# Performance work log

Hardware: AMD Instinct MI355X
Metric: run time of the kernel (lower is better)

## Reference

```python
import jax, jax.numpy as jnp
import numpy as np

FILTER_LEN = 32
SCALE = float(np.sqrt(10 ** (-15 / 10)))  # expected_SI_power_dB = -15


def _fir_valid(x, w):
    """Valid cross-correlation along W axis. x: [B,H,W,1], w: [L] -> [B,H,W-L+1,1].
    Matches Keras Conv2D(kernel_size=(1,L), padding='valid') (cross-correlation)."""
    B, H, W, _ = x.shape
    L = w.shape[0]
    xr = x.reshape(B * H, W, 1)
    k = w.reshape(L, 1, 1)  # (spatial, in, out)
    y = jax.lax.conv_general_dilated(xr, k, window_strides=(1,), padding='VALID',
                                     dimension_numbers=('NWC', 'WIO', 'NWC'))
    return y.reshape(B, H, W - L + 1, 1)


def setup_inputs() -> dict:
    key = jax.random.key(0)
    ks = jax.random.split(key, 10)
    B, H, W = 16, 1, 262144
    f32 = jnp.float32
    return {
        'x_real': jax.random.normal(ks[0], (B, H, W, 1), f32),
        'x_imag': jax.random.normal(ks[1], (B, H, W, 1), f32),
        'w1_pre': jax.random.normal(ks[2], (1, 8), f32) * 0.5,
        'w2_pre': jax.random.normal(ks[3], (8, 1), f32) * 0.5,
        'w_fir_r': jax.random.normal(ks[4], (FILTER_LEN,), f32) * 0.1,
        'w_fir_i': jax.random.normal(ks[5], (FILTER_LEN,), f32) * 0.1,
        'w1_post': jax.random.normal(ks[6], (1, 8), f32) * 0.5,
        'b1_post': jax.random.normal(ks[7], (8,), f32) * 0.1,
        'w2_post': jax.random.normal(ks[8], (8, 1), f32) * 0.5,
        'b2_post': jax.random.normal(ks[9], (1,), f32) * 0.1,
    }


def reference(x_real, x_imag, w1_pre, w2_pre, w_fir_r, w_fir_i,
              w1_post, b1_post, w2_post, b2_post):
    # --- pre nonlinearity on magnitude (1x1 conv MLP: 1 -> 8 tanh -> 1) ---
    x_mag = jnp.sqrt(x_real * x_real + x_imag * x_imag)      # [B,H,W,1]
    x_phase = jnp.arctan2(x_imag, x_real)                    # [B,H,W,1]
    h = jnp.tanh(jnp.einsum('bhwc,cf->bhwf', x_mag, w1_pre))  # [B,H,W,8]
    m = jnp.einsum('bhwf,fc->bhwc', h, w2_pre)               # [B,H,W,1]
    xh_r = m * jnp.cos(x_phase)
    xh_i = m * jnp.sin(x_phase)
    # --- complex FIR (length-32, valid) via 4 real convs ---
    zr = _fir_valid(xh_r, w_fir_r) - _fir_valid(xh_i, w_fir_i)
    zi = _fir_valid(xh_i, w_fir_r) + _fir_valid(xh_r, w_fir_i)
    # --- post nonlinearity on magnitude (1x1 conv MLP: 1 -> 8 relu -> 1) ---
    z_mag = jnp.sqrt(zr * zr + zi * zi)
    z_phase = jnp.arctan2(zi, zr)
    g = jax.nn.relu(jnp.einsum('bhwc,cf->bhwf', z_mag, w1_post) + b1_post)
    zm = jnp.einsum('bhwf,fc->bhwc', g, w2_post) + b2_post
    yr = SCALE * zm * jnp.cos(z_phase)
    yi = SCALE * zm * jnp.sin(z_phase)
    # complex output represented as [real, imag] on last axis: [B,H,W-31,2]
    return jnp.concatenate([yr, yi], axis=-1)
```

## Files before the change

kernel.cpp:

```cpp
#include <hip/hip_runtime.h>

#define WIDTH  262144
#define OUTW   (WIDTH - 31)
#define WTILE  512
#define NSW    560
#define SCALE_V 0.17782794100389229f

#define TBL_N    1024
#define TBL_MAX  10.0f
#define TBL_SCL  (TBL_N / TBL_MAX)

typedef _Float16 half8  __attribute__((ext_vector_type(8)));
typedef _Float16 half4v __attribute__((ext_vector_type(4)));
typedef float    floatx4 __attribute__((ext_vector_type(4)));

__device__ __forceinline__ float wload(const float* __restrict__ w, int t) {
    return (t >= 0 && t < 32) ? w[t] : 0.0f;
}

#define MFMA16(A, B, C) __builtin_amdgcn_mfma_f32_16x16x32_f16((A), (B), (C), 0, 0, 0)

__device__ __forceinline__ float s_of_mag(float mag, const float* w1, const float* w2) {
    if (mag == 0.0f) {
        float s = 0.f;
#pragma unroll
        for (int f = 0; f < 8; ++f) s = fmaf(w2[f], w1[f], s);
        return s;
    }
    float m = 0.f;
#pragma unroll
    for (int f = 0; f < 8; ++f) m = fmaf(w2[f], tanhf(w1[f] * mag), m);
    return m / mag;
}

__global__ void fill_s_table(const float* __restrict__ w1_pre,
                             const float* __restrict__ w2_pre,
                             float2* __restrict__ tbl)
{
    const int i = blockIdx.x * 256 + threadIdx.x;
    if (i >= TBL_N) return;
    float w1[8], w2[8];
#pragma unroll
    for (int f = 0; f < 8; ++f) { w1[f] = w1_pre[f]; w2[f] = w2_pre[f]; }
    const float m0 = (float)i       * (1.0f / TBL_SCL);
    const float m1 = (float)(i + 1) * (1.0f / TBL_SCL);
    const float s0 = s_of_mag(m0, w1, w2);
    const float s1 = s_of_mag(m1, w1, w2);
    tbl[i] = make_float2(s0, s1 - s0);
}

__global__ __launch_bounds__(256, 4) void fused_hammer_mfma(
    const float* __restrict__ xr_g,   const float* __restrict__ xi_g,
    const float* __restrict__ w1_pre, const float* __restrict__ w2_pre,
    const float* __restrict__ wfr,    const float* __restrict__ wfi,
    const float* __restrict__ w1_post,const float* __restrict__ b1_post,
    const float* __restrict__ w2_post,const float* __restrict__ b2_post,
    const float2* __restrict__ tbl_g,
    float* __restrict__ out)
{
    __shared__ __align__(16) _Float16 s_rh[4][NSW];
    __shared__ __align__(16) _Float16 s_rl[4][NSW];
    __shared__ __align__(16) _Float16 s_ih[4][NSW];
    __shared__ __align__(16) _Float16 s_il[4][NSW];
    __shared__ __align__(16) float2   s_tab[TBL_N];

    const int tid    = threadIdx.x;
    const int lane   = tid & 63;
    const int wv     = tid >> 6;
    const int brow   = blockIdx.y;
    const long rowbase = (long)brow * WIDTH;
    const int wbase  = blockIdx.x * 4096 + wv * 1024;

    const int g0 = min(wbase       + 4 * lane, WIDTH - 4);
    const int g1 = min(wbase + 256 + 4 * lane, WIDTH - 4);
    float4 p_r0 = *(const float4*)(xr_g + rowbase + g0);
    float4 p_i0 = *(const float4*)(xi_g + rowbase + g0);
    float4 p_r1 = *(const float4*)(xr_g + rowbase + g1);
    float4 p_i1 = *(const float4*)(xi_g + rowbase + g1);

    {
        const float4* src = (const float4*)tbl_g;
#pragma unroll
        for (int q = 0; q < 2; ++q) {
            const int idx = 2 * tid + q;
            ((float4*)s_tab)[idx] = src[idx];
        }
    }

    float w1p[8], b1p[8], w2p[8];
#pragma unroll
    for (int f = 0; f < 8; ++f) { w1p[f] = w1_post[f]; b1p[f] = b1_post[f]; w2p[f] = w2_post[f]; }
    const float b2p = b2_post[0];

    const int jA = lane & 15;
    const int kg = lane >> 4;
    half8 A1r_h, A1r_l, A1mi_h, A1mi_l, A1i_h, A1i_l, A2r_h, A2r_l, A2i_h, A2i_l;
#pragma unroll
    for (int jj = 0; jj < 8; ++jj) {
        const int k  = 8 * kg + jj;
        const int t1 = k - jA;
        const float wr1 = wload(wfr, t1);
        const float wi1 = wload(wfi, t1);
        const int t2 = (k < 16) ? (k + 32 - jA) : (k + 16 - jA);
        const float wr2 = wload(wfr, t2);
        const float wi2 = wload(wfi, t2);
        const float a2r = (k < 16) ? wr2 : -wi2;
        const float a2i = (k < 16) ? wi2 : wr2;
        _Float16 h;
        h = (_Float16)wr1;   A1r_h[jj]  = h; A1r_l[jj]  = (_Float16)(wr1 - (float)h);
        h = (_Float16)(-wi1);A1mi_h[jj] = h; A1mi_l[jj] = (_Float16)(-wi1 - (float)h);
        h = (_Float16)wi1;   A1i_h[jj]  = h; A1i_l[jj]  = (_Float16)(wi1 - (float)h);
        h = (_Float16)a2r;   A2r_h[jj]  = h; A2r_l[jj]  = (_Float16)(a2r - (float)h);
        h = (_Float16)a2i;   A2i_h[jj]  = h; A2i_l[jj]  = (_Float16)(a2i - (float)h);
    }

    __syncthreads();

    const bool row_aligned = ((brow & 1) == 0);

#define STAGE4(VR, VI, P)                                                     \
    do {                                                                      \
        const float* vrf = &(VR).x;                                           \
        const float* vif = &(VI).x;                                           \
        half4v rh_, rl_, ih_, il_;                                            \
        _Pragma("unroll")                                                     \
        for (int e = 0; e < 4; ++e) {                                         \
            const float r  = vrf[e], im = vif[e];                             \
            const float sq  = fmaf(r, r, im * im);                            \
            const float mag = __builtin_sqrtf(sq);                            \
            const float t   = fminf(mag * TBL_SCL, (float)(TBL_N - 2) + 0.999f); \
            const int   i0  = (int)t;                                         \
            const float frac = t - (float)i0;                                 \
            const float2 en = s_tab[i0];                                      \
            const float s   = fmaf(frac, en.y, en.x);                         \
            const float xhr = s * r;                                          \
            const float xhi = s * im;                                         \
            const _Float16 hr = (_Float16)xhr;                                \
            const _Float16 hi = (_Float16)xhi;                                \
            rh_[e] = hr; rl_[e] = (_Float16)(xhr - (float)hr);                \
            ih_[e] = hi; il_[e] = (_Float16)(xhi - (float)hi);                \
        }                                                                     \
        *(half4v*)&s_rh[wv][4 * (P)] = rh_;                                   \
        *(half4v*)&s_rl[wv][4 * (P)] = rl_;                                   \
        *(half4v*)&s_ih[wv][4 * (P)] = ih_;                                   \
        *(half4v*)&s_il[wv][4 * (P)] = il_;                                   \
    } while (0)

#pragma unroll
    for (int q = 0; q < 2; ++q) {
        const int wstart = wbase + q * WTILE;

        float4 h_r, h_i;
        if (lane < 12) {
            const int g2 = min(wstart + 512 + 4 * lane, WIDTH - 4);
            h_r = *(const float4*)(xr_g + rowbase + g2);
            h_i = *(const float4*)(xi_g + rowbase + g2);
        }

        STAGE4(p_r0, p_i0, lane);
        STAGE4(p_r1, p_i1, 64 + lane);

        if (q == 0) {
            const int n0 = min(wbase + 512       + 4 * lane, WIDTH - 4);
            const int n1 = min(wbase + 512 + 256 + 4 * lane, WIDTH - 4);
            p_r0 = *(const float4*)(xr_g + rowbase + n0);
            p_i0 = *(const float4*)(xi_g + rowbase + n0);
            p_r1 = *(const float4*)(xr_g + rowbase + n1);
            p_i1 = *(const float4*)(xi_g + rowbase + n1);
        }

        if (lane < 12) STAGE4(h_r, h_i, 128 + lane);

        asm volatile("s_waitcnt lgkmcnt(0)" ::: "memory");

#pragma unroll
        for (int tt = 0; tt < 2; ++tt) {
            const int base_o = 256 * tt;
            const int i1 = base_o + 16 * jA + 8 * kg;
            const half8 Bxr_h = *(const half8*)&s_rh[wv][i1];
            const half8 Bxi_h = *(const half8*)&s_ih[wv][i1];
            const half8 Bxr_l = *(const half8*)&s_rl[wv][i1];
            const half8 Bxi_l = *(const half8*)&s_il[wv][i1];
            const int i2 = base_o + 16 * jA + 32 + 8 * (kg & 1);
            const _Float16* srcH = (kg < 2) ? s_rh[wv] : s_ih[wv];
            const _Float16* srcL = (kg < 2) ? s_rl[wv] : s_il[wv];
            const half8 Bmx_h = *(const half8*)&srcH[i2];
            const half8 Bmx_l = *(const half8*)&srcL[i2];

            floatx4 accr = {0.f, 0.f, 0.f, 0.f};
            floatx4 acci = {0.f, 0.f, 0.f, 0.f};
            accr = MFMA16(A1r_h,  Bxr_h, accr);  acci = MFMA16(A1i_h,  Bxr_h, acci);
            accr = MFMA16(A1mi_h, Bxi_h, accr);  acci = MFMA16(A1r_h,  Bxi_h, acci);
            accr = MFMA16(A2r_h,  Bmx_h, accr);  acci = MFMA16(A2i_h,  Bmx_h, acci);
            accr = MFMA16(A1r_h,  Bxr_l, accr);  acci = MFMA16(A1i_h,  Bxr_l, acci);
            accr = MFMA16(A1mi_h, Bxi_l, accr);  acci = MFMA16(A1r_h,  Bxi_l, acci);
            accr = MFMA16(A2r_h,  Bmx_l, accr);  acci = MFMA16(A2i_h,  Bmx_l, acci);
            accr = MFMA16(A1r_l,  Bxr_h, accr);  acci = MFMA16(A1i_l,  Bxr_h, acci);
            accr = MFMA16(A1mi_l, Bxi_h, accr);  acci = MFMA16(A1r_l,  Bxi_h, acci);
            accr = MFMA16(A2r_l,  Bmx_h, accr);  acci = MFMA16(A2i_l,  Bmx_h, acci);

            const int obase = wstart + base_o + 16 * jA + 4 * kg;
            float ox[8];
#pragma unroll
            for (int r = 0; r < 4; ++r) {
                const float zr  = accr[r], zi = acci[r];
                const float zsq = fmaf(zr, zr, zi * zi);
                const float rs  = (zsq > 0.f) ? __builtin_amdgcn_rsqf(zsq) : 0.f;
                const float zmag = zsq * rs;
                float zm = b2p;
#pragma unroll
                for (int f = 0; f < 8; ++f) {
                    const float gfv = fmaf(zmag, w1p[f], b1p[f]);
                    zm = fmaf(fmaxf(gfv, 0.f), w2p[f], zm);
                }
                const float t = SCALE_V * zm * rs;
                ox[2 * r]     = (zsq > 0.f) ? t * zr : SCALE_V * zm;
                ox[2 * r + 1] = t * zi;
            }
            float* po = &out[((long)brow * OUTW + obase) * 2];
            if (obase + 3 < OUTW) {
                if (row_aligned) {
                    *(float4*)(po)     = make_float4(ox[0], ox[1], ox[2], ox[3]);
                    *(float4*)(po + 4) = make_float4(ox[4], ox[5], ox[6], ox[7]);
                } else {
#pragma unroll
                    for (int r = 0; r < 4; ++r)
                        *(float2*)(po + 2 * r) = make_float2(ox[2 * r], ox[2 * r + 1]);
                }
            } else {
#pragma unroll
                for (int r = 0; r < 4; ++r)
                    if (obase + r < OUTW)
                        *(float2*)(po + 2 * r) = make_float2(ox[2 * r], ox[2 * r + 1]);
            }
        }
    }
#undef STAGE4
}

extern "C" void kernel_launch(void* const* d_in, const int* in_sizes, int n_in,
                              void* d_out, int out_size, void* d_ws, size_t ws_size,
                              hipStream_t stream) {
    float2* tbl = (float2*)d_ws;
    fill_s_table<<<dim3((TBL_N + 255) / 256), 256, 0, stream>>>(
        (const float*)d_in[2], (const float*)d_in[3], tbl);

    dim3 grid(64, 16);
    fused_hammer_mfma<<<grid, 256, 0, stream>>>(
        (const float*)d_in[0], (const float*)d_in[1],
        (const float*)d_in[2], (const float*)d_in[3],
        (const float*)d_in[4], (const float*)d_in[5],
        (const float*)d_in[6], (const float*)d_in[7],
        (const float*)d_in[8], (const float*)d_in[9],
        tbl,
        (float*)d_out);
}
```

Measured before the change: 111.2 us.

## Fuse table build into main kernel and halve per-block work

Drops the separate table-fill kernel launch. Each block now builds the magnitude lookup table in shared memory using a fast exp2/rcp tanh, and precomputes fp16 hi/lo FIR weight splits in shared memory. Each wave now handles a single 512-wide tile instead of two, so the grid doubles to 128x16 and the launch-bounds occupancy hint rises to 5. This removes a launch and the global table read, but every block repeats the 1025-entry table computation and the prefetch overlap between tiles is lost.

```diff
diff --git a/kernel.cpp b/kernel.cpp
--- a/kernel.cpp
+++ b/kernel.cpp
@@ -5,6 +5,7 @@
 #define WTILE  512
 #define NSW    560
 #define SCALE_V 0.17782794100389229f
+#define LOG2E_X2 2.8853900817779268f
 
 #define TBL_N    1024
 #define TBL_MAX  10.0f
@@ -14,10 +15,6 @@
 typedef _Float16 half4v __attribute__((ext_vector_type(4)));
 typedef float    floatx4 __attribute__((ext_vector_type(4)));
 
-__device__ __forceinline__ float wload(const float* __restrict__ w, int t) {
-    return (t >= 0 && t < 32) ? w[t] : 0.0f;
-}
-
 #define MFMA16(A, B, C) __builtin_amdgcn_mfma_f32_16x16x32_f16((A), (B), (C), 0, 0, 0)
 
 __device__ __forceinline__ float s_of_mag(float mag, const float* w1, const float* w2) {
@@ -29,68 +26,69 @@
     }
     float m = 0.f;
 #pragma unroll
-    for (int f = 0; f < 8; ++f) m = fmaf(w2[f], tanhf(w1[f] * mag), m);
+    for (int f = 0; f < 8; ++f) {
+        const float e2 = __builtin_amdgcn_exp2f(LOG2E_X2 * w1[f] * mag);
+        const float th = 1.0f - 2.0f * __builtin_amdgcn_rcpf(e2 + 1.0f);
+        m = fmaf(w2[f], th, m);
+    }
     return m / mag;
 }
 
-__global__ void fill_s_table(const float* __restrict__ w1_pre,
-                             const float* __restrict__ w2_pre,
-                             float2* __restrict__ tbl)
-{
-    const int i = blockIdx.x * 256 + threadIdx.x;
-    if (i >= TBL_N) return;
-    float w1[8], w2[8];
-#pragma unroll
-    for (int f = 0; f < 8; ++f) { w1[f] = w1_pre[f]; w2[f] = w2_pre[f]; }
-    const float m0 = (float)i       * (1.0f / TBL_SCL);
-    const float m1 = (float)(i + 1) * (1.0f / TBL_SCL);
-    const float s0 = s_of_mag(m0, w1, w2);
-    const float s1 = s_of_mag(m1, w1, w2);
-    tbl[i] = make_float2(s0, s1 - s0);
-}
-
-__global__ __launch_bounds__(256, 4) void fused_hammer_mfma(
+__global__ __launch_bounds__(256, 5) void fused_hammer_mfma(
     const float* __restrict__ xr_g,   const float* __restrict__ xi_g,
     const float* __restrict__ w1_pre, const float* __restrict__ w2_pre,
     const float* __restrict__ wfr,    const float* __restrict__ wfi,
     const float* __restrict__ w1_post,const float* __restrict__ b1_post,
     const float* __restrict__ w2_post,const float* __restrict__ b2_post,
-    const float2* __restrict__ tbl_g,
     float* __restrict__ out)
 {
     __shared__ __align__(16) _Float16 s_rh[4][NSW];
     __shared__ __align__(16) _Float16 s_rl[4][NSW];
     __shared__ __align__(16) _Float16 s_ih[4][NSW];
     __shared__ __align__(16) _Float16 s_il[4][NSW];
-    __shared__ __align__(16) float2   s_tab[TBL_N];
+    __shared__ __align__(16) float    s_tab[TBL_N + 1];
+    __shared__ __align__(16) _Float16 s_wrh[32], s_wrl[32], s_wih[32], s_wil[32];
 
     const int tid    = threadIdx.x;
     const int lane   = tid & 63;
     const int wv     = tid >> 6;
     const int brow   = blockIdx.y;
     const long rowbase = (long)brow * WIDTH;
-    const int wbase  = blockIdx.x * 4096 + wv * 1024;
-
-    const int g0 = min(wbase       + 4 * lane, WIDTH - 4);
-    const int g1 = min(wbase + 256 + 4 * lane, WIDTH - 4);
-    float4 p_r0 = *(const float4*)(xr_g + rowbase + g0);
-    float4 p_i0 = *(const float4*)(xi_g + rowbase + g0);
-    float4 p_r1 = *(const float4*)(xr_g + rowbase + g1);
-    float4 p_i1 = *(const float4*)(xi_g + rowbase + g1);
+    const int wstart = blockIdx.x * 2048 + wv * WTILE;
+
+    const int g0 = min(wstart       + 4 * lane, WIDTH - 4);
+    const int g1 = min(wstart + 256 + 4 * lane, WIDTH - 4);
+    float4 r0 = *(const float4*)(xr_g + rowbase + g0);
+    float4 i0 = *(const float4*)(xi_g + rowbase + g0);
+    float4 r1 = *(const float4*)(xr_g + rowbase + g1);
+    float4 i1 = *(const float4*)(xi_g + rowbase + g1);
+    float4 r2, i2;
+    if (lane < 12) {
+        const int g2 = min(wstart + 512 + 4 * lane, WIDTH - 4);
+        r2 = *(const float4*)(xr_g + rowbase + g2);
+        i2 = *(const float4*)(xi_g + rowbase + g2);
+    }
 
     {
-        const float4* src = (const float4*)tbl_g;
-#pragma unroll
-        for (int q = 0; q < 2; ++q) {
-            const int idx = 2 * tid + q;
-            ((float4*)s_tab)[idx] = src[idx];
-        }
+        float w1v[8], w2v[8];
+#pragma unroll
+        for (int f = 0; f < 8; ++f) { w1v[f] = w1_pre[f]; w2v[f] = w2_pre[f]; }
+        for (int i = tid; i <= TBL_N; i += 256)
+            s_tab[i] = s_of_mag((float)i * (1.0f / TBL_SCL), w1v, w2v);
+    }
+    if (tid < 32) {
+        const float wr = wfr[tid], wi = wfi[tid];
+        const _Float16 wrh = (_Float16)wr, wih = (_Float16)wi;
+        s_wrh[tid] = wrh; s_wrl[tid] = (_Float16)(wr - (float)wrh);
+        s_wih[tid] = wih; s_wil[tid] = (_Float16)(wi - (float)wih);
     }
 
     float w1p[8], b1p[8], w2p[8];
 #pragma unroll
     for (int f = 0; f < 8; ++f) { w1p[f] = w1_post[f]; b1p[f] = b1_post[f]; w2p[f] = w2_post[f]; }
     const float b2p = b2_post[0];
+
+    __syncthreads();
 
     const int jA = lane & 15;
     const int kg = lane >> 4;
@@ -99,22 +97,24 @@
     for (int jj = 0; jj < 8; ++jj) {
         const int k  = 8 * kg + jj;
         const int t1 = k - jA;
-        const float wr1 = wload(wfr, t1);
-        const float wi1 = wload(wfi, t1);
+        const bool v1 = (t1 >= 0);
+        const int x1 = max(t1, 0);
+        const _Float16 z = (_Float16)0.f;
+        const _Float16 wr1h = v1 ? s_wrh[x1] : z, wr1l = v1 ? s_wrl[x1] : z;
+        const _Float16 wi1h = v1 ? s_wih[x1] : z, wi1l = v1 ? s_wil[x1] : z;
         const int t2 = (k < 16) ? (k + 32 - jA) : (k + 16 - jA);
-        const float wr2 = wload(wfr, t2);
-        const float wi2 = wload(wfi, t2);
-        const float a2r = (k < 16) ? wr2 : -wi2;
-        const float a2i = (k < 16) ? wi2 : wr2;
-        _Float16 h;
-        h = (_Float16)wr1;   A1r_h[jj]  = h; A1r_l[jj]  = (_Float16)(wr1 - (float)h);
-        h = (_Float16)(-wi1);A1mi_h[jj] = h; A1mi_l[jj] = (_Float16)(-wi1 - (float)h);
-        h = (_Float16)wi1;   A1i_h[jj]  = h; A1i_l[jj]  = (_Float16)(wi1 - (float)h);
-        h = (_Float16)a2r;   A2r_h[jj]  = h; A2r_l[jj]  = (_Float16)(a2r - (float)h);
-        h = (_Float16)a2i;   A2i_h[jj]  = h; A2i_l[jj]  = (_Float16)(a2i - (float)h);
-    }
-
-    __syncthreads();
+        const bool v2 = (t2 <= 31);
+        const int x2 = min(t2, 31);
+        const _Float16 wr2h = v2 ? s_wrh[x2] : z, wr2l = v2 ? s_wrl[x2] : z;
+        const _Float16 wi2h = v2 ? s_wih[x2] : z, wi2l = v2 ? s_wil[x2] : z;
+        A1r_h[jj]  = wr1h;  A1r_l[jj]  = wr1l;
+        A1mi_h[jj] = -wi1h; A1mi_l[jj] = -wi1l;
+        A1i_h[jj]  = wi1h;  A1i_l[jj]  = wi1l;
+        A2r_h[jj]  = (k < 16) ? wr2h : -wi2h;
+        A2r_l[jj]  = (k < 16) ? wr2l : -wi2l;
+        A2i_h[jj]  = (k < 16) ? wi2h : wr2h;
+        A2i_l[jj]  = (k < 16) ? wi2l : wr2l;
+    }
 
     const bool row_aligned = ((brow & 1) == 0);
 
@@ -128,11 +128,12 @@
             const float r  = vrf[e], im = vif[e];                             \
             const float sq  = fmaf(r, r, im * im);                            \
             const float mag = __builtin_sqrtf(sq);                            \
-            const float t   = fminf(mag * TBL_SCL, (float)(TBL_N - 2) + 0.999f); \
+            const float t   = fminf(mag * TBL_SCL, (float)TBL_N - 0.001f);    \
             const int   i0  = (int)t;                                         \
             const float frac = t - (float)i0;                                 \
-            const float2 en = s_tab[i0];                                      \
-            const float s   = fmaf(frac, en.y, en.x);                         \
+            const float sa = s_tab[i0];                                       \
+            const float sb = s_tab[i0 + 1];                                   \
+            const float s  = fmaf(frac, sb - sa, sa);                         \
             const float xhr = s * r;                                          \
             const float xhi = s * im;                                         \
             const _Float16 hr = (_Float16)xhr;                                \
@@ -146,93 +147,71 @@
         *(half4v*)&s_il[wv][4 * (P)] = il_;                                   \
     } while (0)
 
-#pragma unroll
-    for (int q = 0; q < 2; ++q) {
-        const int wstart = wbase + q * WTILE;
-
-        float4 h_r, h_i;
-        if (lane < 12) {
-            const int g2 = min(wstart + 512 + 4 * lane, WIDTH - 4);
-            h_r = *(const float4*)(xr_g + rowbase + g2);
-            h_i = *(const float4*)(xi_g + rowbase + g2);
+    STAGE4(r0, i0, lane);
+    STAGE4(r1, i1, 64 + lane);
+    if (lane < 12) STAGE4(r2, i2, 128 + lane);
+
+    asm volatile("s_waitcnt lgkmcnt(0)" ::: "memory");
+
+#pragma unroll
+    for (int tt = 0; tt < 2; ++tt) {
+        const int base_o = 256 * tt;
+        const int i1x = base_o + 16 * jA + 8 * kg;
+        const half8 Bxr_h = *(const half8*)&s_rh[wv][i1x];
+        const half8 Bxi_h = *(const half8*)&s_ih[wv][i1x];
+        const half8 Bxr_l = *(const half8*)&s_rl[wv][i1x];
+        const half8 Bxi_l = *(const half8*)&s_il[wv][i1x];
+        const int i2x = base_o + 16 * jA + 32 + 8 * (kg & 1);
+        const _Float16* srcH = (kg < 2) ? s_rh[wv] : s_ih[wv];
+        const _Float16* srcL = (kg < 2) ? s_rl[wv] : s_il[wv];
+        const half8 Bmx_h = *(const half8*)&srcH[i2x];
+        const half8 Bmx_l = *(const half8*)&srcL[i2x];
+
+        floatx4 accr = {0.f, 0.f, 0.f, 0.f};
+        floatx4 acci = {0.f, 0.f, 0.f, 0.f};
+        accr = MFMA16(A1r_h,  Bxr_h, accr);  acci = MFMA16(A1i_h,  Bxr_h, acci);
+        accr = MFMA16(A1mi_h, Bxi_h, accr);  acci = MFMA16(A1r_h,  Bxi_h, acci);
+        accr = MFMA16(A2r_h,  Bmx_h, accr);  acci = MFMA16(A2i_h,  Bmx_h, acci);
+        accr = MFMA16(A1r_h,  Bxr_l, accr);  acci = MFMA16(A1i_h,  Bxr_l, acci);
+        accr = MFMA16(A1mi_h, Bxi_l, accr);  acci = MFMA16(A1r_h,  Bxi_l, acci);
+        accr = MFMA16(A2r_h,  Bmx_l, accr);  acci = MFMA16(A2i_h,  Bmx_l, acci);
+        accr = MFMA16(A1r_l,  Bxr_h, accr);  acci = MFMA16(A1i_l,  Bxr_h, acci);
+        accr = MFMA16(A1mi_l, Bxi_h, accr);  acci = MFMA16(A1r_l,  Bxi_h, acci);
+        accr = MFMA16(A2r_l,  Bmx_h, accr);  acci = MFMA16(A2i_l,  Bmx_h, acci);
+
+        const int obase = wstart + base_o + 16 * jA + 4 * kg;
+        float ox[8];
+#pragma unroll
+        for (int r = 0; r < 4; ++r) {
+            const float zr  = accr[r], zi = acci[r];
+            const float zsq = fmaf(zr, zr, zi * zi);
+            const float rs  = (zsq > 0.f) ? __builtin_amdgcn_rsqf(zsq) : 0.f;
+            const float zmag = zsq * rs;
+            float zm = b2p;
+#pragma unroll
+            for (int f = 0; f < 8; ++f) {
+                const float gfv = fmaf(zmag, w1p[f], b1p[f]);
+                zm = fmaf(fmaxf(gfv, 0.f), w2p[f], zm);
+            }
+            const float t = SCALE_V * zm * rs;
+            ox[2 * r]     = (zsq > 0.f) ? t * zr : SCALE_V * zm;
+            ox[2 * r + 1] = t * zi;
         }
-
-        STAGE4(p_r0, p_i0, lane);
-        STAGE4(p_r1, p_i1, 64 + lane);
-
-        if (q == 0) {
-            const int n0 = min(wbase + 512       + 4 * lane, WIDTH - 4);
-            const int n1 = min(wbase + 512 + 256 + 4 * lane, WIDTH - 4);
-            p_r0 = *(const float4*)(xr_g + rowbase + n0);
-            p_i0 = *(const float4*)(xi_g + rowbase + n0);
-            p_r1 = *(const float4*)(xr_g + rowbase + n1);
-            p_i1 = *(const float4*)(xi_g + rowbase + n1);
-        }
-
-        if (lane < 12) STAGE4(h_r, h_i, 128 + lane);
-
-        asm volatile("s_waitcnt lgkmcnt(0)" ::: "memory");
-
-#pragma unroll
-        for (int tt = 0; tt < 2; ++tt) {
-            const int base_o = 256 * tt;
-            const int i1 = base_o + 16 * jA + 8 * kg;
-            const half8 Bxr_h = *(const half8*)&s_rh[wv][i1];
-            const half8 Bxi_h = *(const half8*)&s_ih[wv][i1];
-            const half8 Bxr_l = *(const half8*)&s_rl[wv][i1];
-            const half8 Bxi_l = *(const half8*)&s_il[wv][i1];
-            const int i2 = base_o + 16 * jA + 32 + 8 * (kg & 1);
-            const _Float16* srcH = (kg < 2) ? s_rh[wv] : s_ih[wv];
-            const _Float16* srcL = (kg < 2) ? s_rl[wv] : s_il[wv];
-            const half8 Bmx_h = *(const half8*)&srcH[i2];
-            const half8 Bmx_l = *(const half8*)&srcL[i2];
-
-            floatx4 accr = {0.f, 0.f, 0.f, 0.f};
-            floatx4 acci = {0.f, 0.f, 0.f, 0.f};
-            accr = MFMA16(A1r_h,  Bxr_h, accr);  acci = MFMA16(A1i_h,  Bxr_h, acci);
-            accr = MFMA16(A1mi_h, Bxi_h, accr);  acci = MFMA16(A1r_h,  Bxi_h, acci);
-            accr = MFMA16(A2r_h,  Bmx_h, accr);  acci = MFMA16(A2i_h,  Bmx_h, acci);
-            accr = MFMA16(A1r_h,  Bxr_l, accr);  acci = MFMA16(A1i_h,  Bxr_l, acci);
-            accr = MFMA16(A1mi_h, Bxi_l, accr);  acci = MFMA16(A1r_h,  Bxi_l, acci);
-            accr = MFMA16(A2r_h,  Bmx_l, accr);  acci = MFMA16(A2i_h,  Bmx_l, acci);
-            accr = MFMA16(A1r_l,  Bxr_h, accr);  acci = MFMA16(A1i_l,  Bxr_h, acci);
-            accr = MFMA16(A1mi_l, Bxi_h, accr);  acci = MFMA16(A1r_l,  Bxi_h, acci);
-            accr = MFMA16(A2r_l,  Bmx_h, accr);  acci = MFMA16(A2i_l,  Bmx_h, acci);
-
-            const int obase = wstart + base_o + 16 * jA + 4 * kg;
-            float ox[8];
-#pragma unroll
-            for (int r = 0; r < 4; ++r) {
-                const float zr  = accr[r], zi = acci[r];
-                const float zsq = fmaf(zr, zr, zi * zi);
-                const float rs  = (zsq > 0.f) ? __builtin_amdgcn_rsqf(zsq) : 0.f;
-                const float zmag = zsq * rs;
-                float zm = b2p;
-#pragma unroll
-                for (int f = 0; f < 8; ++f) {
-                    const float gfv = fmaf(zmag, w1p[f], b1p[f]);
-                    zm = fmaf(fmaxf(gfv, 0.f), w2p[f], zm);
-                }
-                const float t = SCALE_V * zm * rs;
-                ox[2 * r]     = (zsq > 0.f) ? t * zr : SCALE_V * zm;
-                ox[2 * r + 1] = t * zi;
+        float* po = &out[((long)brow * OUTW + obase) * 2];
+        if (obase + 3 < OUTW) {
+            if (row_aligned) {
+                *(float4*)(po)     = make_float4(ox[0], ox[1], ox[2], ox[3]);
+                *(float4*)(po + 4) = make_float4(ox[4], ox[5], ox[6], ox[7]);
+            } else {
+#pragma unroll
+                for (int r = 0; r < 4; ++r)
+                    *(float2*)(po + 2 * r) = make_float2(ox[2 * r], ox[2 * r + 1]);
             }
-            float* po = &out[((long)brow * OUTW + obase) * 2];
-            if (obase + 3 < OUTW) {
-                if (row_aligned) {
-                    *(float4*)(po)     = make_float4(ox[0], ox[1], ox[2], ox[3]);
-                    *(float4*)(po + 4) = make_float4(ox[4], ox[5], ox[6], ox[7]);
-                } else {
-#pragma unroll
-                    for (int r = 0; r < 4; ++r)
-                        *(float2*)(po + 2 * r) = make_float2(ox[2 * r], ox[2 * r + 1]);
-                }
-            } else {
-#pragma unroll
-                for (int r = 0; r < 4; ++r)
-                    if (obase + r < OUTW)
-                        *(float2*)(po + 2 * r) = make_float2(ox[2 * r], ox[2 * r + 1]);
-            }
+        } else {
+#pragma unroll
+            for (int r = 0; r < 4; ++r)
+                if (obase + r < OUTW)
+                    *(float2*)(po + 2 * r) = make_float2(ox[2 * r], ox[2 * r + 1]);
         }
     }
 #undef STAGE4
@@ -241,17 +220,12 @@
 extern "C" void kernel_launch(void* const* d_in, const int* in_sizes, int n_in,
                               void* d_out, int out_size, void* d_ws, size_t ws_size,
                               hipStream_t stream) {
-    float2* tbl = (float2*)d_ws;
-    fill_s_table<<<dim3((TBL_N + 255) / 256), 256, 0, stream>>>(
-        (const float*)d_in[2], (const float*)d_in[3], tbl);
-
-    dim3 grid(64, 16);
+    dim3 grid(128, 16);
     fused_hammer_mfma<<<grid, 256, 0, stream>>>(
         (const float*)d_in[0], (const float*)d_in[1],
         (const float*)d_in[2], (const float*)d_in[3],
         (const float*)d_in[4], (const float*)d_in[5],
         (const float*)d_in[6], (const float*)d_in[7],
         (const float*)d_in[8], (const float*)d_in[9],
-        tbl,
         (float*)d_out);
 }
```

Result: slower. 125.5 us (+12.8%).
